# Kernel tuning notes

Measured on AMD Instinct MI355X. Metric: run time of the kernel, lower is better.

## Reference

```python
import jax, jax.numpy as jnp
import numpy as np

B, F, D = 2048, 40, 32
CIN = (64, 64)


def _glorot(key, shape):
    fan_in, fan_out = shape[1] * shape[2], shape[0] * shape[2]
    std = jnp.sqrt(2.0 / (fan_in + fan_out)).astype(jnp.float32)
    return jax.random.normal(key, shape, dtype=jnp.float32) * std


def setup_inputs() -> dict:
    key = jax.random.key(0)
    kx, k0, k1 = jax.random.split(key, 3)
    x = jax.random.normal(kx, (B, F, D), dtype=jnp.float32)
    W0 = _glorot(k0, (CIN[0], F * F, D))
    b0 = jnp.zeros((CIN[0],), dtype=jnp.float32)
    W1 = _glorot(k1, (CIN[1], F * CIN[0], D))
    b1 = jnp.zeros((CIN[1],), dtype=jnp.float32)
    return {"x": x, "W0": W0, "b0": b0, "W1": W1, "b1": b1}


def _cin_step(x0, xk, W, b):
    # x0: (B,F,D)  xk: (B,H,D)  W: (O, H*F, D)  b: (O,)
    Bn, H, Dn = xk.shape
    Fn = x0.shape[1]
    # outer product per embedding channel, h-major flatten as in tf.reshape
    z = jnp.einsum('bhd,bfd->bhfd', xk, x0).reshape(Bn, H * Fn, Dn)
    # per-embedding-channel contraction against weights: (B,D,O)
    y = jnp.einsum('bhd,ohd->bdo', z, W) + b
    y = jax.nn.relu(y)
    return jnp.transpose(y, (0, 2, 1))  # (B,O,D)


def reference(x, W0, b0, W1, b1):
    x1 = _cin_step(x, x, W0, b0)
    x2 = _cin_step(x, x1, W1, b1)
    final = jnp.concatenate([x, x1, x2], axis=1)  # (B, F+O0+O1, D)
    return jnp.sum(final, axis=-1)  # (B, F+O0+O1)
```

## Files before the change

### kernel.cpp

```cpp
#include <hip/hip_runtime.h>

typedef unsigned int   u32;
typedef unsigned short u16;
typedef _Float16       f16;

using f16x8  = __attribute__((ext_vector_type(8)))  _Float16;
using f16x2  = __attribute__((ext_vector_type(2)))  _Float16;
using f32x16 = __attribute__((ext_vector_type(16))) float;

#define KEEP(x) asm volatile("" : "+v"(x))

__global__ __launch_bounds__(256)
void prep(const float* __restrict__ x,
          const float* __restrict__ W0, const float* __restrict__ W1,
          f16* __restrict__ xt, f16* __restrict__ W0p, f16* __restrict__ W1p,
          float* __restrict__ out){
  __shared__ char shm[33920];
  const int tid = threadIdx.x;
  if (blockIdx.x < 2560){
    float (*tile)[33] = (float(*)[33])shm;
    const int r0 = blockIdx.x << 5;
    const int c  = tid & 31;
    const int rp = tid >> 5;
#pragma unroll
    for (int p = 0; p < 4; ++p){
      const int r = (p << 3) + rp;
      float v = x[(size_t)(r0 + r) * 32 + c];
      tile[r][c] = v;
      float s = v;
#pragma unroll
      for (int off = 16; off > 0; off >>= 1) s += __shfl_xor(s, off, 32);
      if (c == 0){
        const int row = r0 + r;
        out[(size_t)(row / 40) * 168 + (row % 40)] = s;
      }
    }
    __syncthreads();
#pragma unroll
    for (int p = 0; p < 4; ++p){
      const int dd = (p << 3) + rp;
      xt[(size_t)dd * 81920 + r0 + c] = (f16)tile[c][dd];
    }
  } else {
    u16* t = (u16*)shm;
    int kb = blockIdx.x - 2560;
    const float* in; f16* outp; int K;
    if (kb < 200){ in = W0; outp = W0p; K = 1600; }
    else         { kb -= 200; in = W1; outp = W1p; K = 2560; }
    const int kbase = kb << 3;
#pragma unroll 4
    for (int i = 0; i < 64; ++i){
      const int idx = tid + (i << 8);
      const int o   = idx >> 8;
      const int rem = idx & 255;
      const int e   = rem >> 5;
      const int dd  = rem & 31;
      const float v = in[(size_t)o * (K * 32) + (size_t)(kbase + e) * 32 + dd];
      union { f16 h; u16 u; } cv; cv.h = (f16)v;
      t[dd * 530 + o * 8 + e] = cv.u;
    }
    __syncthreads();
    const u32* t32 = (const u32*)t;
    u32* o32 = (u32*)outp;
    const int obase = kb << 8;
#pragma unroll 4
    for (int i = 0; i < 32; ++i){
      const int idx = tid + (i << 8);
      const int dd  = idx >> 8;
      const int rem = idx & 255;
      o32[(size_t)dd * (K * 32) + obase + rem] = t32[dd * 265 + rem];
    }
  }
}

__global__ __launch_bounds__(256, 2)
void cin_fused(const f16* __restrict__ xt,
               const f16* __restrict__ W0p,
               const f16* __restrict__ W1p,
               const float* __restrict__ b0v, const float* __restrict__ b1v,
               f16* __restrict__ x1s,
               f16* __restrict__ y2s){
  constexpr int XOFF = 16896;

  const int bid = blockIdx.x;
  const int d   = ((bid & 7) << 2) | ((bid >> 3) & 3);
  const int b0  = (bid >> 5) << 6;
  const int tid = threadIdx.x;
  const int wv  = tid >> 6;
  const int kh  = wv >> 1;
  const int wc  = wv & 1;
  const int l   = tid & 63;
  const int hi  = l >> 5;
  const int lr  = l & 31;

  __shared__ char smem[26112];

  const f16* gW0 = W0p + (size_t)d * 102400;
  const f16* gW1 = W1p + (size_t)d * 163840;
  const int lane_off = hi * 512 + ((wc << 5) + lr) * 8;

  f16x8 B0[5], B1[5];

#define LOADB(B, GP, TT) do { \
    _Pragma("unroll") \
    for (int mi_ = 0; mi_ < 5; ++mi_) \
      (B)[mi_] = *(const f16x8*)((GP) + (size_t)(TT) * 5120 + mi_ * 1024); \
    __builtin_amdgcn_sched_barrier(0); \
  } while (0)

  const f16* g1 = gW0 + kh * 51200 + lane_off;
  LOADB(B0, g1, 0);

  {
    const uint4* src = (const uint4*)(xt + (size_t)d * 81920 + (size_t)b0 * 40);
#pragma unroll
    for (int it = 0; it < 2; ++it){
      const int idx = tid + (it << 8);
      if (idx < 320){
        const int r = idx / 5, c = idx - r * 5;
        *(uint4*)(smem + XOFF + r * 96 + c * 16) = src[idx];
      }
    }
  }
  __syncthreads();

  const char* x0row = smem + XOFF + lr * 96;
  const char* x1row = smem + XOFF + lr * 144;
  const int   col = (wc << 5) + lr;
  const float bv1 = b0v[col];
  const float bv2 = b1v[col];

  f16x8 sl[2][5];
#pragma unroll
  for (int m = 0; m < 2; ++m){
    const char* xe = x0row + m * 3072 + hi * 16;
#pragma unroll
    for (int t = 0; t < 4; ++t) sl[m][t] = *(const f16x8*)(xe + t * 16);
    sl[m][4] = *(const f16x8*)(x0row + m * 3072 + (hi ? 0 : 64));
  }
  KEEP(sl[0][0]); KEEP(sl[0][1]); KEEP(sl[0][2]); KEEP(sl[0][3]); KEEP(sl[0][4]);
  KEEP(sl[1][0]); KEEP(sl[1][1]); KEEP(sl[1][2]); KEEP(sl[1][3]); KEEP(sl[1][4]);

  const f32x16 fz = {0,0,0,0,0,0,0,0,0,0,0,0,0,0,0,0};
  f32x16 accA = fz, accB = fz;

  static constexpr int SI[5] = {0, 2, 4, 1, 3};

#define COMP(B, XB, TT, HOFF, MS) do { \
    const f16x2 xhp0 = *(const f16x2*)((XB) + (HOFF) + (TT) * 4); \
    const f16x2 xhp1 = *(const f16x2*)((XB) + (HOFF) + (TT) * 4 + (MS)); \
    __builtin_amdgcn_s_setprio(1); \
    _Pragma("unroll") \
    for (int mi = 0; mi < 5; ++mi){ \
      const f16x8 bf = (B)[mi]; \
      const f16 xa0 = (mi < 2) ? xhp0[0] : (mi > 2) ? xhp0[1] : (hi ? xhp0[1] : xhp0[0]); \
      const f16 xa1 = (mi < 2) ? xhp1[0] : (mi > 2) ? xhp1[1] : (hi ? xhp1[1] : xhp1[0]); \
      accA = __builtin_amdgcn_mfma_f32_32x32x16_f16(sl[0][SI[mi]] * xa0, bf, accA, 0, 0, 0); \
      accB = __builtin_amdgcn_mfma_f32_32x32x16_f16(sl[1][SI[mi]] * xa1, bf, accB, 0, 0, 0); \
    } \
    __builtin_amdgcn_s_setprio(0); \
  } while (0)

  {
    const int hoff = kh * 40;
    for (int t = 0; t < 10; t += 2){
      LOADB(B1, g1, t + 1);
      COMP(B0, x0row, t, hoff, 3072);
      LOADB(B0, g1, t + 2);
      COMP(B1, x0row, t + 1, hoff, 3072);
    }
  }

  float* redp = (float*)(smem + wc * 8448);
  u16*   x1w  = (u16*)(smem + XOFF);
  if (kh == 1){
#pragma unroll
    for (int m = 0; m < 2; ++m)
#pragma unroll
      for (int reg = 0; reg < 16; ++reg){
        const int row = (m << 5) + (reg & 3) + ((reg >> 2) << 3) + (hi << 2);
        redp[row * 33 + lr] = (m ? accB[reg] : accA[reg]);
      }
  }
  __syncthreads();
  if (kh == 0){
#pragma unroll
    for (int m = 0; m < 2; ++m)
#pragma unroll
      for (int reg = 0; reg < 16; ++reg){
        const int row = (m << 5) + (reg & 3) + ((reg >> 2) << 3) + (hi << 2);
        float v = (m ? accB[reg] : accA[reg]) + redp[row * 33 + lr] + bv1;
        v = v > 0.f ? v : 0.f;
        union { f16 h; u16 u; } cv; cv.h = (f16)v;
        x1w[row * 72 + col] = cv.u;
      }
  }
  accA = fz; accB = fz;
  const f16* g2 = gW1 + kh * 81920 + lane_off;
  LOADB(B0, g2, 0);
  __syncthreads();

  {
#pragma unroll
    for (int it = 0; it < 2; ++it){
      const int u   = tid + (it << 8);
      const int row = u >> 3, ch = u & 7;
      const f16x8 vv = *(const f16x8*)((const char*)x1w + row * 144 + ch * 16);
      *(f16x8*)(x1s + (size_t)(b0 + row) * 2048 + d * 64 + ch * 8) = vv;
    }
  }

  {
    const int hoff = kh * 64;
    for (int t = 0; t < 16; t += 2){
      LOADB(B1, g2, t + 1);
      COMP(B0, x1row, t, hoff, 4608);
      LOADB(B0, g2, t + 2);
      COMP(B1, x1row, t + 1, hoff, 4608);
    }
  }

  if (kh == 1){
#pragma unroll
    for (int m = 0; m < 2; ++m)
#pragma unroll
      for (int reg = 0; reg < 16; ++reg){
        const int row = (m << 5) + (reg & 3) + ((reg >> 2) << 3) + (hi << 2);
        redp[row * 33 + lr] = (m ? accB[reg] : accA[reg]);
      }
  }
  __syncthreads();
  if (kh == 0){
#pragma unroll
    for (int m = 0; m < 2; ++m)
#pragma unroll
      for (int reg = 0; reg < 16; ++reg){
        const int row = (m << 5) + (reg & 3) + ((reg >> 2) << 3) + (hi << 2);
        float v = (m ? accB[reg] : accA[reg]) + redp[row * 33 + lr] + bv2;
        v = v > 0.f ? v : 0.f;
        union { f16 h; u16 u; } cv; cv.h = (f16)v;
        x1w[row * 72 + col] = cv.u;
      }
  }
  __syncthreads();
  {
#pragma unroll
    for (int it = 0; it < 2; ++it){
      const int u   = tid + (it << 8);
      const int row = u >> 3, ch = u & 7;
      const f16x8 vv = *(const f16x8*)((const char*)x1w + row * 144 + ch * 16);
      *(f16x8*)(y2s + (size_t)(b0 + row) * 2048 + d * 64 + ch * 8) = vv;
    }
  }
#undef LOADB
#undef COMP
}

__global__ __launch_bounds__(128)
void finalize(const f16* __restrict__ x1s, const f16* __restrict__ y2s,
              float* __restrict__ out){
  const int b = blockIdx.x;
  const int t = threadIdx.x;
  if (t < 64){
    float s = 0.f;
#pragma unroll
    for (int d = 0; d < 32; ++d) s += (float)x1s[(size_t)b * 2048 + d * 64 + t];
    out[(size_t)b * 168 + 40 + t] = s;
  } else {
    const int o = t - 64;
    float s = 0.f;
#pragma unroll
    for (int d = 0; d < 32; ++d) s += (float)y2s[(size_t)b * 2048 + d * 64 + o];
    out[(size_t)b * 168 + 104 + o] = s;
  }
}

extern "C" void kernel_launch(void* const* d_in, const int* in_sizes, int n_in,
                              void* d_out, int out_size, void* d_ws, size_t ws_size,
                              hipStream_t stream){
  const float* x   = (const float*)d_in[0];
  const float* W0  = (const float*)d_in[1];
  const float* b0v = (const float*)d_in[2];
  const float* W1  = (const float*)d_in[3];
  const float* b1v = (const float*)d_in[4];
  float* out = (float*)d_out;

  char* ws = (char*)d_ws;
  f16* xt  = (f16*)(ws + 0);
  f16* W0p = (f16*)(ws + 5242880);
  f16* W1p = (f16*)(ws + 11796480);
  f16* x1s = (f16*)(ws + 22282240);
  f16* y2s = (f16*)(ws + 30670848);

  prep<<<3080, 256, 0, stream>>>(x, W0, W1, xt, W0p, W1p, out);
  cin_fused<<<1024, 256, 0, stream>>>(xt, W0p, W1p, b0v, b1v, x1s, y2s);
  finalize<<<2048, 128, 0, stream>>>(x1s, y2s, out);
}
```

Measured before the change: 62.87 us.

## Preload per-row x scalars into registers and fully unroll MFMA loops

The per-step LDS reads of the x_h scalars are replaced by loading each lane's row of x0/x1 into registers once before each stage. Both stage loops are fully unrolled, the sched_barrier and setprio hints are removed, and the first W1 tile prefetch moves ahead of the stage-1 reduction. The goal is to cut LDS traffic and latency inside the MFMA loop and to let the compiler interleave global loads with MFMAs. The cost is higher register pressure and less explicit control over scheduling.

Result: faster. 60.50 us (-3.8%).

```diff
diff --git a/kernel.cpp b/kernel.cpp
--- a/kernel.cpp
+++ b/kernel.cpp
@@ -5,7 +5,7 @@
 typedef _Float16       f16;
 
 using f16x8  = __attribute__((ext_vector_type(8)))  _Float16;
-using f16x2  = __attribute__((ext_vector_type(2)))  _Float16;
+using f16x4  = __attribute__((ext_vector_type(4)))  _Float16;
 using f32x16 = __attribute__((ext_vector_type(16))) float;
 
 #define KEEP(x) asm volatile("" : "+v"(x))
@@ -99,17 +99,16 @@
   const f16* gW1 = W1p + (size_t)d * 163840;
   const int lane_off = hi * 512 + ((wc << 5) + lr) * 8;
 
-  f16x8 B0[5], B1[5];
+  f16x8 Ba[5], Bb[5];
 
 #define LOADB(B, GP, TT) do { \
     _Pragma("unroll") \
     for (int mi_ = 0; mi_ < 5; ++mi_) \
       (B)[mi_] = *(const f16x8*)((GP) + (size_t)(TT) * 5120 + mi_ * 1024); \
-    __builtin_amdgcn_sched_barrier(0); \
   } while (0)
 
   const f16* g1 = gW0 + kh * 51200 + lane_off;
-  LOADB(B0, g1, 0);
+  LOADB(Ba, g1, 0);
 
   {
     const uint4* src = (const uint4*)(xt + (size_t)d * 81920 + (size_t)b0 * 40);
@@ -141,35 +140,41 @@
   KEEP(sl[0][0]); KEEP(sl[0][1]); KEEP(sl[0][2]); KEEP(sl[0][3]); KEEP(sl[0][4]);
   KEEP(sl[1][0]); KEEP(sl[1][1]); KEEP(sl[1][2]); KEEP(sl[1][3]); KEEP(sl[1][4]);
 
+  f16x4 xq0[5], xq1[5];
+#pragma unroll
+  for (int q = 0; q < 5; ++q){
+    xq0[q] = *(const f16x4*)(x0row + kh * 40 + q * 8);
+    xq1[q] = *(const f16x4*)(x0row + 3072 + kh * 40 + q * 8);
+    KEEP(xq0[q]); KEEP(xq1[q]);
+  }
+
   const f32x16 fz = {0,0,0,0,0,0,0,0,0,0,0,0,0,0,0,0};
   f32x16 accA = fz, accB = fz;
 
   static constexpr int SI[5] = {0, 2, 4, 1, 3};
 
-#define COMP(B, XB, TT, HOFF, MS) do { \
-    const f16x2 xhp0 = *(const f16x2*)((XB) + (HOFF) + (TT) * 4); \
-    const f16x2 xhp1 = *(const f16x2*)((XB) + (HOFF) + (TT) * 4 + (MS)); \
-    __builtin_amdgcn_s_setprio(1); \
-    _Pragma("unroll") \
-    for (int mi = 0; mi < 5; ++mi){ \
-      const f16x8 bf = (B)[mi]; \
-      const f16 xa0 = (mi < 2) ? xhp0[0] : (mi > 2) ? xhp0[1] : (hi ? xhp0[1] : xhp0[0]); \
-      const f16 xa1 = (mi < 2) ? xhp1[0] : (mi > 2) ? xhp1[1] : (hi ? xhp1[1] : xhp1[0]); \
-      accA = __builtin_amdgcn_mfma_f32_32x32x16_f16(sl[0][SI[mi]] * xa0, bf, accA, 0, 0, 0); \
-      accB = __builtin_amdgcn_mfma_f32_32x32x16_f16(sl[1][SI[mi]] * xa1, bf, accB, 0, 0, 0); \
-    } \
-    __builtin_amdgcn_s_setprio(0); \
-  } while (0)
-
-  {
-    const int hoff = kh * 40;
-    for (int t = 0; t < 10; t += 2){
-      LOADB(B1, g1, t + 1);
-      COMP(B0, x0row, t, hoff, 3072);
-      LOADB(B0, g1, t + 2);
-      COMP(B1, x0row, t + 1, hoff, 3072);
-    }
-  }
+#pragma unroll
+  for (int t = 0; t < 10; ++t){
+    if (t + 1 < 10){
+      if ((t + 1) & 1) { LOADB(Bb, g1, t + 1); } else { LOADB(Ba, g1, t + 1); }
+    }
+    const int e0 = 2 * t, e1 = 2 * t + 1;
+    const f16 a_lo = xq0[e0 >> 2][e0 & 3], a_hi = xq0[e1 >> 2][e1 & 3];
+    const f16 b_lo = xq1[e0 >> 2][e0 & 3], b_hi = xq1[e1 >> 2][e1 & 3];
+    const f16 am = hi ? a_hi : a_lo;
+    const f16 bm = hi ? b_hi : b_lo;
+#pragma unroll
+    for (int mi = 0; mi < 5; ++mi){
+      const f16x8 bf = ((t & 1) ? Bb : Ba)[mi];
+      const f16 xa0 = (mi < 2) ? a_lo : (mi > 2) ? a_hi : am;
+      const f16 xa1 = (mi < 2) ? b_lo : (mi > 2) ? b_hi : bm;
+      accA = __builtin_amdgcn_mfma_f32_32x32x16_f16(sl[0][SI[mi]] * xa0, bf, accA, 0, 0, 0);
+      accB = __builtin_amdgcn_mfma_f32_32x32x16_f16(sl[1][SI[mi]] * xa1, bf, accB, 0, 0, 0);
+    }
+  }
+
+  const f16* g2 = gW1 + kh * 81920 + lane_off;
+  LOADB(Ba, g2, 0);
 
   float* redp = (float*)(smem + wc * 8448);
   u16*   x1w  = (u16*)(smem + XOFF);
@@ -196,8 +201,6 @@
       }
   }
   accA = fz; accB = fz;
-  const f16* g2 = gW1 + kh * 81920 + lane_off;
-  LOADB(B0, g2, 0);
   __syncthreads();
 
   {
@@ -210,13 +213,31 @@
     }
   }
 
-  {
-    const int hoff = kh * 64;
-    for (int t = 0; t < 16; t += 2){
-      LOADB(B1, g2, t + 1);
-      COMP(B0, x1row, t, hoff, 4608);
-      LOADB(B0, g2, t + 2);
-      COMP(B1, x1row, t + 1, hoff, 4608);
+  f16x8 xk0[4], xk1[4];
+#pragma unroll
+  for (int q = 0; q < 4; ++q){
+    xk0[q] = *(const f16x8*)(x1row + kh * 64 + q * 16);
+    xk1[q] = *(const f16x8*)(x1row + 4608 + kh * 64 + q * 16);
+    KEEP(xk0[q]); KEEP(xk1[q]);
+  }
+
+#pragma unroll
+  for (int t = 0; t < 16; ++t){
+    if (t + 1 < 16){
+      if ((t + 1) & 1) { LOADB(Bb, g2, t + 1); } else { LOADB(Ba, g2, t + 1); }
+    }
+    const int e0 = 2 * t, e1 = 2 * t + 1;
+    const f16 a_lo = xk0[e0 >> 3][e0 & 7], a_hi = xk0[e1 >> 3][e1 & 7];
+    const f16 b_lo = xk1[e0 >> 3][e0 & 7], b_hi = xk1[e1 >> 3][e1 & 7];
+    const f16 am = hi ? a_hi : a_lo;
+    const f16 bm = hi ? b_hi : b_lo;
+#pragma unroll
+    for (int mi = 0; mi < 5; ++mi){
+      const f16x8 bf = ((t & 1) ? Bb : Ba)[mi];
+      const f16 xa0 = (mi < 2) ? a_lo : (mi > 2) ? a_hi : am;
+      const f16 xa1 = (mi < 2) ? b_lo : (mi > 2) ? b_hi : bm;
+      accA = __builtin_amdgcn_mfma_f32_32x32x16_f16(sl[0][SI[mi]] * xa0, bf, accA, 0, 0, 0);
+      accB = __builtin_amdgcn_mfma_f32_32x32x16_f16(sl[1][SI[mi]] * xa1, bf, accB, 0, 0, 0);
     }
   }
 
@@ -253,7 +274,6 @@
     }
   }
 #undef LOADB
-#undef COMP
 }
 
 __global__ __launch_bounds__(128)
```
